# Kernel tuning notes

Measured on AMD Instinct MI355X. Metric: run time of the kernel, lower is better.

The kernel has to match this reference:

```python
import jax, jax.numpy as jnp
import numpy as np
import math

H, W, K = 512, 512, 256
EPS = 1e-6


def _make_grid(H, W):
    # Faithful to make_coord_grid: grid[a, b] = (xs[a], ys[b]) after the
    # torch meshgrid('xy') + permute(1,0,2) dance. With H == W this is (H, W, 2).
    xs = jnp.linspace(-1.0, 1.0, W)
    ys = jnp.linspace(-1.0, 1.0, H)
    X, Y = jnp.meshgrid(xs, ys, indexing='ij')  # (W, H)
    return jnp.stack([X, Y], axis=-1)  # (W, H, 2) == (H, W, 2) here


def setup_inputs() -> dict:
    key = jax.random.key(0)
    k_mu, k_theta, k_color = jax.random.split(key, 3)
    grid = _make_grid(H, W).astype(jnp.float32)
    mu = jax.random.uniform(k_mu, (K, 2), minval=-0.8, maxval=0.8, dtype=jnp.float32)
    log_scales = jnp.full((K, 2), math.log(0.3), dtype=jnp.float32)
    theta = jax.random.uniform(k_theta, (K,), minval=-math.pi, maxval=math.pi, dtype=jnp.float32)
    color_logits = 0.5 * jax.random.normal(k_color, (K, 3), dtype=jnp.float32)
    log_amp = jnp.full((K, 1), math.log(0.5), dtype=jnp.float32)
    return {
        'grid': grid,
        'mu': mu,
        'log_scales': log_scales,
        'theta': theta,
        'color_logits': color_logits,
        'log_amp': log_amp,
    }


def reference(grid, mu, log_scales, theta, color_logits, log_amp):
    scales = jnp.exp(log_scales)                      # (K, 2)
    sx, sy = scales[:, 0], scales[:, 1]
    # per-pixel, per-Gaussian offsets: (H, W, K)
    dx = grid[:, :, None, 0] - mu[None, None, :, 0]
    dy = grid[:, :, None, 1] - mu[None, None, :, 1]
    c, s = jnp.cos(theta), jnp.sin(theta)
    vx = dx * c + dy * s
    vy = -dx * s + dy * c
    q = vx * vx / (sx * sx + EPS) + vy * vy / (sy * sy + EPS)
    G = jnp.exp(-0.5 * q)                             # (H, W, K)
    amp = jax.nn.softplus(log_amp)[:, 0]              # (K,)
    weights = G * amp
    colors = jax.nn.sigmoid(color_logits)             # (K, 3)
    num = jnp.einsum('hwk,kc->hwc', weights, colors)  # (H, W, 3)
    den = jnp.sum(weights, axis=-1, keepdims=True)    # (H, W, 1)
    img = jnp.clip(num / (den + EPS), 0.0, 1.0)
    return img
```

## Files before the change

kernel.cpp:

```cpp
#include <hip/hip_runtime.h>
#include <hip/hip_bf16.h>
#include <math.h>

#define HH   512
#define WW   512
#define KG   256
#define EPSF 1e-6f
#define LOG2E 1.4426950408889634f
#define DGRID (32.0f / 511.0f)

typedef short bf16x8 __attribute__((ext_vector_type(8)));
typedef float f32x4  __attribute__((ext_vector_type(4)));

union FragU { unsigned u[4]; bf16x8 v; };

__device__ __forceinline__ unsigned pkbf(float a, float b) {
    unsigned r;
    asm("v_cvt_pk_bf16_f32 %0, %1, %2" : "=v"(r) : "v"(a), "v"(b));
    return r;
}

#define SIDX(k) ((((k) & 7) << 5) + ((k) >> 3))

__global__ __launch_bounds__(512, 2) void gauss_render(
    const float* __restrict__ grid,
    const float* __restrict__ mu,
    const float* __restrict__ log_scales,
    const float* __restrict__ theta,
    const float* __restrict__ color_logits,
    const float* __restrict__ log_amp,
    float* __restrict__ out)
{
    __shared__ float4 sA[KG];
    __shared__ float4 sC[KG];
    __shared__ uint4  pkA4[8 * 17];
    __shared__ float  sY[WW];

    const int tid = threadIdx.x;
    const int col = blockIdx.x;

    const float2 p = reinterpret_cast<const float2*>(grid)[col * WW + tid];
    sY[tid] = p.y;
    const float X = p.x;

    if (tid < KG) {
        const int k = tid;
        const float mx  = mu[2 * k + 0];
        const float my  = mu[2 * k + 1];
        const float sx  = expf(log_scales[2 * k + 0]);
        const float sy  = expf(log_scales[2 * k + 1]);
        const float isx = 1.0f / (sx * sx + EPSF);
        const float isy = 1.0f / (sy * sy + EPSF);
        const float t   = theta[k];
        const float c   = cosf(t);
        const float s   = sinf(t);

        const float A = c * c * isx + s * s * isy;
        const float B = s * s * isx + c * c * isy;
        const float C = 2.0f * c * s * (isx - isy);

        const float la  = log_amp[k];
        const float amp = (la > 20.0f) ? la : log1pf(expf(la));
        const float lnA = logf(amp);

        const float ca = -0.5f * LOG2E * A;
        const float cb = -0.5f * LOG2E * B;
        const float cc = -0.5f * LOG2E * C;
        const float cd = LOG2E * (A * mx + 0.5f * C * my);
        const float ce = LOG2E * (B * my + 0.5f * C * mx);
        const float cf = LOG2E * (lnA - 0.5f * (A * mx * mx + B * my * my + C * mx * my));

        const float c0 = 1.0f / (1.0f + expf(-color_logits[3 * k + 0]));
        const float c1 = 1.0f / (1.0f + expf(-color_logits[3 * k + 1]));
        const float c2 = 1.0f / (1.0f + expf(-color_logits[3 * k + 2]));

        const float b1 = fmaf(cc, X, ce);
        const float b0 = fmaf(fmaf(ca, X, cd), X, cf);
        const float cr = __builtin_amdgcn_exp2f(2.0f * cb * DGRID * DGRID);

        sA[SIDX(k)] = make_float4(b0, b1, cb, cr);
        sC[k]       = make_float4(c0 - 0.5f, c1 - 0.5f, c2 - 0.5f, 1.0f);
    }
    __syncthreads();

    if (tid < 128) {
        const int m  = tid;
        const int kt = m >> 4, g = (m >> 2) & 3, i = m & 3;
        unsigned* pw = reinterpret_cast<unsigned*>(pkA4);
        #pragma unroll
        for (int ch = 0; ch < 4; ++ch) {
            const unsigned v = pkbf(((const float*)&sC[2 * m    ])[ch],
                                    ((const float*)&sC[2 * m + 1])[ch]);
            pw[(kt * 17 + ch * 4 + g) * 4 + i] = v;
        }
    }
    if (tid < 8) pkA4[tid * 17 + 16] = make_uint4(0u, 0u, 0u, 0u);
    __syncthreads();

    const int lane = tid & 63;
    const int wv   = tid >> 6;
    const int cidx = lane & 15;
    const int g    = lane >> 4;
    const int aOff = (cidx < 4) ? (cidx * 4 + g) : 16;

    const float Y0  = sY[wv * 64 + cidx];
    const float Y2D = 2.0f * Y0 + DGRID;

    f32x4 acc0 = {0.f,0.f,0.f,0.f}, acc1 = {0.f,0.f,0.f,0.f};
    f32x4 acc2 = {0.f,0.f,0.f,0.f}, acc3 = {0.f,0.f,0.f,0.f};

    #pragma unroll 1
    for (int kt = 0; kt < 8; ++kt) {
        const int bk = kt * 32 + g * 8;

        FragU af;
        {
            const uint4 av = pkA4[kt * 17 + aOff];
            af.u[0] = av.x; af.u[1] = av.y; af.u[2] = av.z; af.u[3] = av.w;
        }

        FragU b0f, b1f, b2f, b3f;
        #pragma unroll
        for (int i = 0; i < 4; ++i) {
            const int k0 = bk + 2 * i;
            const float4 q0 = sA[SIDX(k0)];
            const float4 q1 = sA[SIDX(k0 + 1)];

            const float e0a = fmaf(fmaf(q0.z, Y0, q0.y), Y0, q0.x);
            const float dta = DGRID * fmaf(q0.z, Y2D, q0.y);
            float       ra  = __builtin_amdgcn_exp2f(dta);
            const float w0a = __builtin_amdgcn_exp2f(e0a);
            const float w1a = w0a * ra;  ra *= q0.w;
            const float w2a = w1a * ra;  ra *= q0.w;
            const float w3a = w2a * ra;

            const float e0b = fmaf(fmaf(q1.z, Y0, q1.y), Y0, q1.x);
            const float dtb = DGRID * fmaf(q1.z, Y2D, q1.y);
            float       rb  = __builtin_amdgcn_exp2f(dtb);
            const float w0b = __builtin_amdgcn_exp2f(e0b);
            const float w1b = w0b * rb;  rb *= q1.w;
            const float w2b = w1b * rb;  rb *= q1.w;
            const float w3b = w2b * rb;

            b0f.u[i] = pkbf(w0a, w0b);
            b1f.u[i] = pkbf(w1a, w1b);
            b2f.u[i] = pkbf(w2a, w2b);
            b3f.u[i] = pkbf(w3a, w3b);
        }

        acc0 = __builtin_amdgcn_mfma_f32_16x16x32_bf16(af.v, b0f.v, acc0, 0, 0, 0);
        acc1 = __builtin_amdgcn_mfma_f32_16x16x32_bf16(af.v, b1f.v, acc1, 0, 0, 0);
        acc2 = __builtin_amdgcn_mfma_f32_16x16x32_bf16(af.v, b2f.v, acc2, 0, 0, 0);
        acc3 = __builtin_amdgcn_mfma_f32_16x16x32_bf16(af.v, b3f.v, acc3, 0, 0, 0);
    }

    if (lane < 16) {
        #pragma unroll
        for (int t = 0; t < 4; ++t) {
            const f32x4 acc = (t == 0) ? acc0 : (t == 1) ? acc1 : (t == 2) ? acc2 : acc3;
            const int pix = col * WW + (wv * 4 + t) * 16 + lane;
            const float inv = 1.0f / (acc[3] + EPSF);
            const float r   = fmaf(0.5f, acc[3], acc[0]) * inv;
            const float gch = fmaf(0.5f, acc[3], acc[1]) * inv;
            const float bch = fmaf(0.5f, acc[3], acc[2]) * inv;
            out[3 * pix + 0] = fminf(fmaxf(r,   0.0f), 1.0f);
            out[3 * pix + 1] = fminf(fmaxf(gch, 0.0f), 1.0f);
            out[3 * pix + 2] = fminf(fmaxf(bch, 0.0f), 1.0f);
        }
    }
}

extern "C" void kernel_launch(void* const* d_in, const int* in_sizes, int n_in,
                              void* d_out, int out_size, void* d_ws, size_t ws_size,
                              hipStream_t stream) {
    const float* grid         = (const float*)d_in[0];
    const float* mu           = (const float*)d_in[1];
    const float* log_scales   = (const float*)d_in[2];
    const float* theta        = (const float*)d_in[3];
    const float* color_logits = (const float*)d_in[4];
    const float* log_amp      = (const float*)d_in[5];
    float* out = (float*)d_out;

    const int threads = 512;
    const int blocks  = HH;
    hipLaunchKernelGGL(gauss_render, dim3(blocks), dim3(threads), 0, stream,
                       grid, mu, log_scales, theta, color_logits, log_amp, out);
}
```

Baseline: 15.50 us.

## Halve block size and compute eight pixel tiles per wave

The block shrinks from 512 to 256 threads, so each wave now covers 128 rows (eight 16-pixel tiles) instead of 64. Each wave computes a second Gaussian exp2 seed at Y4 and extends the multiplicative recurrence to eight weights per Gaussian. Per-block setup (parameter precompute, shared tables) and the A-fragment loads are amortised over more pixels, and exp2 calls per pixel drop. In exchange the kernel uses more registers (eight accumulators and eight B fragments), has fewer waves in flight, and the longer multiplicative chain may add bf16 rounding error.

```diff
diff --git a/kernel.cpp b/kernel.cpp
--- a/kernel.cpp
+++ b/kernel.cpp
@@ -22,7 +22,7 @@
 
 #define SIDX(k) ((((k) & 7) << 5) + ((k) >> 3))
 
-__global__ __launch_bounds__(512, 2) void gauss_render(
+__global__ __launch_bounds__(256, 2) void gauss_render(
     const float* __restrict__ grid,
     const float* __restrict__ mu,
     const float* __restrict__ log_scales,
@@ -39,11 +39,14 @@
     const int tid = threadIdx.x;
     const int col = blockIdx.x;
 
-    const float2 p = reinterpret_cast<const float2*>(grid)[col * WW + tid];
-    sY[tid] = p.y;
-    const float X = p.x;
-
-    if (tid < KG) {
+    const float2* g2 = reinterpret_cast<const float2*>(grid);
+    const float2 pA = g2[col * WW + tid];
+    const float2 pB = g2[col * WW + tid + 256];
+    sY[tid]       = pA.y;
+    sY[tid + 256] = pB.y;
+    const float X = pA.x;
+
+    {
         const int k = tid;
         const float mx  = mu[2 * k + 0];
         const float my  = mu[2 * k + 1];
@@ -103,11 +106,14 @@
     const int g    = lane >> 4;
     const int aOff = (cidx < 4) ? (cidx * 4 + g) : 16;
 
-    const float Y0  = sY[wv * 64 + cidx];
+    const float Y0  = sY[wv * 128 + cidx];
+    const float Y4  = sY[wv * 128 + 64 + cidx];
     const float Y2D = 2.0f * Y0 + DGRID;
 
     f32x4 acc0 = {0.f,0.f,0.f,0.f}, acc1 = {0.f,0.f,0.f,0.f};
     f32x4 acc2 = {0.f,0.f,0.f,0.f}, acc3 = {0.f,0.f,0.f,0.f};
+    f32x4 acc4 = {0.f,0.f,0.f,0.f}, acc5 = {0.f,0.f,0.f,0.f};
+    f32x4 acc6 = {0.f,0.f,0.f,0.f}, acc7 = {0.f,0.f,0.f,0.f};
 
     #pragma unroll 1
     for (int kt = 0; kt < 8; ++kt) {
@@ -119,54 +125,88 @@
             af.u[0] = av.x; af.u[1] = av.y; af.u[2] = av.z; af.u[3] = av.w;
         }
 
-        FragU b0f, b1f, b2f, b3f;
+        FragU b0f, b1f, b2f, b3f, b4f, b5f, b6f, b7f;
         #pragma unroll
         for (int i = 0; i < 4; ++i) {
             const int k0 = bk + 2 * i;
             const float4 q0 = sA[SIDX(k0)];
             const float4 q1 = sA[SIDX(k0 + 1)];
 
-            const float e0a = fmaf(fmaf(q0.z, Y0, q0.y), Y0, q0.x);
-            const float dta = DGRID * fmaf(q0.z, Y2D, q0.y);
-            float       ra  = __builtin_amdgcn_exp2f(dta);
-            const float w0a = __builtin_amdgcn_exp2f(e0a);
-            const float w1a = w0a * ra;  ra *= q0.w;
-            const float w2a = w1a * ra;  ra *= q0.w;
-            const float w3a = w2a * ra;
-
-            const float e0b = fmaf(fmaf(q1.z, Y0, q1.y), Y0, q1.x);
-            const float dtb = DGRID * fmaf(q1.z, Y2D, q1.y);
-            float       rb  = __builtin_amdgcn_exp2f(dtb);
-            const float w0b = __builtin_amdgcn_exp2f(e0b);
-            const float w1b = w0b * rb;  rb *= q1.w;
-            const float w2b = w1b * rb;  rb *= q1.w;
-            const float w3b = w2b * rb;
-
-            b0f.u[i] = pkbf(w0a, w0b);
-            b1f.u[i] = pkbf(w1a, w1b);
-            b2f.u[i] = pkbf(w2a, w2b);
-            b3f.u[i] = pkbf(w3a, w3b);
+            const float dta  = DGRID * fmaf(q0.z, Y2D, q0.y);
+            const float e0a  = fmaf(fmaf(q0.z, Y0, q0.y), Y0, q0.x);
+            const float e4a  = fmaf(fmaf(q0.z, Y4, q0.y), Y4, q0.x);
+            const float ca1  = q0.w;
+            const float ca2  = ca1 * ca1;
+            const float ra   = __builtin_amdgcn_exp2f(dta);
+            const float rca  = ra * ca1;
+            const float rca2 = ra * ca2;
+            const float r4a  = rca2 * ca2;
+            const float r4ca = r4a * ca1;
+            const float r4ca2= r4a * ca2;
+            const float wa0  = __builtin_amdgcn_exp2f(e0a);
+            const float wa4  = __builtin_amdgcn_exp2f(e4a);
+            const float wa1  = wa0 * ra;
+            const float wa2  = wa1 * rca;
+            const float wa3  = wa2 * rca2;
+            const float wa5  = wa4 * r4a;
+            const float wa6  = wa5 * r4ca;
+            const float wa7  = wa6 * r4ca2;
+
+            const float dtb  = DGRID * fmaf(q1.z, Y2D, q1.y);
+            const float e0b  = fmaf(fmaf(q1.z, Y0, q1.y), Y0, q1.x);
+            const float e4b  = fmaf(fmaf(q1.z, Y4, q1.y), Y4, q1.x);
+            const float cb1  = q1.w;
+            const float cb2  = cb1 * cb1;
+            const float rb   = __builtin_amdgcn_exp2f(dtb);
+            const float rcb  = rb * cb1;
+            const float rcb2 = rb * cb2;
+            const float r4b  = rcb2 * cb2;
+            const float r4cb = r4b * cb1;
+            const float r4cb2= r4b * cb2;
+            const float wb0  = __builtin_amdgcn_exp2f(e0b);
+            const float wb4  = __builtin_amdgcn_exp2f(e4b);
+            const float wb1  = wb0 * rb;
+            const float wb2  = wb1 * rcb;
+            const float wb3  = wb2 * rcb2;
+            const float wb5  = wb4 * r4b;
+            const float wb6  = wb5 * r4cb;
+            const float wb7  = wb6 * r4cb2;
+
+            b0f.u[i] = pkbf(wa0, wb0);
+            b1f.u[i] = pkbf(wa1, wb1);
+            b2f.u[i] = pkbf(wa2, wb2);
+            b3f.u[i] = pkbf(wa3, wb3);
+            b4f.u[i] = pkbf(wa4, wb4);
+            b5f.u[i] = pkbf(wa5, wb5);
+            b6f.u[i] = pkbf(wa6, wb6);
+            b7f.u[i] = pkbf(wa7, wb7);
         }
 
         acc0 = __builtin_amdgcn_mfma_f32_16x16x32_bf16(af.v, b0f.v, acc0, 0, 0, 0);
         acc1 = __builtin_amdgcn_mfma_f32_16x16x32_bf16(af.v, b1f.v, acc1, 0, 0, 0);
         acc2 = __builtin_amdgcn_mfma_f32_16x16x32_bf16(af.v, b2f.v, acc2, 0, 0, 0);
         acc3 = __builtin_amdgcn_mfma_f32_16x16x32_bf16(af.v, b3f.v, acc3, 0, 0, 0);
+        acc4 = __builtin_amdgcn_mfma_f32_16x16x32_bf16(af.v, b4f.v, acc4, 0, 0, 0);
+        acc5 = __builtin_amdgcn_mfma_f32_16x16x32_bf16(af.v, b5f.v, acc5, 0, 0, 0);
+        acc6 = __builtin_amdgcn_mfma_f32_16x16x32_bf16(af.v, b6f.v, acc6, 0, 0, 0);
+        acc7 = __builtin_amdgcn_mfma_f32_16x16x32_bf16(af.v, b7f.v, acc7, 0, 0, 0);
     }
 
     if (lane < 16) {
-        #pragma unroll
-        for (int t = 0; t < 4; ++t) {
-            const f32x4 acc = (t == 0) ? acc0 : (t == 1) ? acc1 : (t == 2) ? acc2 : acc3;
-            const int pix = col * WW + (wv * 4 + t) * 16 + lane;
-            const float inv = 1.0f / (acc[3] + EPSF);
-            const float r   = fmaf(0.5f, acc[3], acc[0]) * inv;
-            const float gch = fmaf(0.5f, acc[3], acc[1]) * inv;
-            const float bch = fmaf(0.5f, acc[3], acc[2]) * inv;
-            out[3 * pix + 0] = fminf(fmaxf(r,   0.0f), 1.0f);
-            out[3 * pix + 1] = fminf(fmaxf(gch, 0.0f), 1.0f);
-            out[3 * pix + 2] = fminf(fmaxf(bch, 0.0f), 1.0f);
-        }
+        #define EPI(ACC, T)                                                     \
+        {                                                                       \
+            const int pix = col * WW + (wv * 8 + (T)) * 16 + lane;              \
+            const float inv = 1.0f / ((ACC)[3] + EPSF);                         \
+            const float r   = fmaf(0.5f, (ACC)[3], (ACC)[0]) * inv;             \
+            const float gch = fmaf(0.5f, (ACC)[3], (ACC)[1]) * inv;             \
+            const float bch = fmaf(0.5f, (ACC)[3], (ACC)[2]) * inv;             \
+            out[3 * pix + 0] = fminf(fmaxf(r,   0.0f), 1.0f);                   \
+            out[3 * pix + 1] = fminf(fmaxf(gch, 0.0f), 1.0f);                   \
+            out[3 * pix + 2] = fminf(fmaxf(bch, 0.0f), 1.0f);                   \
+        }
+        EPI(acc0, 0) EPI(acc1, 1) EPI(acc2, 2) EPI(acc3, 3)
+        EPI(acc4, 4) EPI(acc5, 5) EPI(acc6, 6) EPI(acc7, 7)
+        #undef EPI
     }
 }
 
@@ -181,7 +221,7 @@
     const float* log_amp      = (const float*)d_in[5];
     float* out = (float*)d_out;
 
-    const int threads = 512;
+    const int threads = 256;
     const int blocks  = HH;
     hipLaunchKernelGGL(gauss_render, dim3(blocks), dim3(threads), 0, stream,
                        grid, mu, log_scales, theta, color_logits, log_amp, out);
```

After: 16.10 us. 1.04x slower.
